# Optimization experiments

Measured on AMD Instinct MI355X. Metric: run time of the kernel, lower is better.

## Reference

```python
import jax, jax.numpy as jnp
import numpy as np

NUM_LAYERS = 2


def setup_inputs() -> dict:
    key = jax.random.key(0)
    ks = jax.random.split(key, 8)
    B, S, I, H = 64, 512, 64, 512
    def lin(kw, kb, fan_in, fan_out):
        bound = 1.0 / np.sqrt(fan_in)
        W = jax.random.uniform(kw, (fan_in, fan_out), jnp.float32, -bound, bound)
        b = jax.random.uniform(kb, (fan_out,), jnp.float32, -bound, bound)
        return W, b
    W0, b0 = lin(ks[0], ks[1], I + H, 4 * H)      # layer 0: cat(x_t, h0) -> gates
    W1, b1 = lin(ks[2], ks[3], H + H, 4 * H)      # layer 1: cat(h0, h1) -> gates
    Wfc, bfc = lin(ks[4], ks[5], H, 1)            # output head
    x = jax.random.normal(ks[6], (B, S, I), jnp.float32)
    return {"x": x, "W0": W0, "b0": b0, "W1": W1, "b1": b1, "Wfc": Wfc, "bfc": bfc}


def _lstm_cell(inp, h, c, W, b):
    gates = jnp.concatenate([inp, h], axis=1) @ W + b   # [B, 4H]
    i, f, g, o = jnp.split(gates, 4, axis=1)             # torch chunk order: i,f,g,o
    c_next = jax.nn.sigmoid(f) * c + jax.nn.sigmoid(i) * jnp.tanh(g)
    h_next = jax.nn.sigmoid(o) * jnp.tanh(c_next)
    return h_next, c_next


def reference(x, W0, b0, W1, b1, Wfc, bfc):
    B, S, _ = x.shape
    H = W0.shape[1] // 4
    Ws, bs = (W0, W1), (b0, b1)
    h0 = jnp.zeros((NUM_LAYERS, B, H), x.dtype)
    c0 = jnp.zeros((NUM_LAYERS, B, H), x.dtype)

    def step(carry, xt):
        h, c = carry
        hs, cs = [], []
        inp = xt
        for l in range(NUM_LAYERS):
            hn, cn = _lstm_cell(inp, h[l], c[l], Ws[l], bs[l])
            hs.append(hn); cs.append(cn)
            inp = hn
        return (jnp.stack(hs), jnp.stack(cs)), None

    (h_fin, _), _ = jax.lax.scan(step, (h0, c0), jnp.swapaxes(x, 0, 1))
    # original applies fc to every timestep then keeps only the last ->
    # equivalent to fc on final top-layer hidden state
    pred = h_fin[-1] @ Wfc + bfc    # [B, 1]
    return pred[:, 0]               # squeeze -> [B]
```

## Files before the change

kernel.cpp:

```cpp
#include <hip/hip_runtime.h>

#define S_LEN 512
#define HID   512
#define IN_D  64
#define GATES 2048
#define K0    576
#define K1    1024
#define KP0   578
#define KP1   1026
#define CLUSTERS 4
#define WGS   64
#define BPC   16
#define NBLOCKS 256
#define NTHREADS 256
#define NPROD 128u

typedef _Float16 f16;
typedef _Float16 f16x8 __attribute__((ext_vector_type(8)));
typedef float    f32x4 __attribute__((ext_vector_type(4)));

#define LDS_W0_OFF  0
#define LDS_W1_OFF  (32 * KP0 * 2)
#define LDS_STG_OFF (LDS_W1_OFF + 32 * KP1 * 2)
#define LDS_TOTAL   (LDS_STG_OFF + 4 * 16 * 17 * 4)

#define WS_FLAG_BYTES 65536
#define SLOT_BYTES    32768

#define RELEASE_DRAIN() asm volatile("s_waitcnt vmcnt(0) lgkmcnt(0)" ::: "memory")
#define MFMA(a,b,c) __builtin_amdgcn_mfma_f32_16x16x32_f16((a),(b),(c),0,0,0)

__device__ __forceinline__ float sigf(float v) {
  v = fminf(fmaxf(v, -30.f), 30.f);
  return 1.f / (1.f + __expf(-v));
}
__device__ __forceinline__ float tanh_f(float v) {
  v = fminf(fmaxf(v, -15.f), 15.f);
  float e = __expf(2.f * v);
  return (e - 1.f) / (e + 1.f);
}

__device__ __forceinline__ void wait_cnt(const unsigned* p, unsigned need, int& budget) {
  for (;;) {
    unsigned v = __hip_atomic_load(p, __ATOMIC_RELAXED, __HIP_MEMORY_SCOPE_AGENT);
    if (v >= need) break;
    if (--budget < 0) break;
    __builtin_amdgcn_s_sleep(1);
  }
  asm volatile("" ::: "memory");
}

extern "C" __global__ void __launch_bounds__(NTHREADS, 1)
lstm_persist(const float* __restrict__ x,  const float* __restrict__ W0,
             const float* __restrict__ b0, const float* __restrict__ W1,
             const float* __restrict__ b1, const float* __restrict__ Wfc,
             const float* __restrict__ bfc, float* __restrict__ out,
             unsigned char* __restrict__ ws, int Wn, int wmask, int fimask, int slack)
{
  extern __shared__ char lds[];
  f16*   w0l     = (f16*)(lds + LDS_W0_OFF);
  f16*   w1l     = (f16*)(lds + LDS_W1_OFF);
  float* stgbase = (float*)(lds + LDS_STG_OFF);

  const int tid   = threadIdx.x;
  const int wg    = blockIdx.x & (WGS - 1);
  const int cl    = blockIdx.x / WGS;
  const int wave  = tid >> 6;
  const int lane  = tid & 63;
  const int hbase = wg * 8;

  {
    const int nl = tid & 31;
    const int wtile = nl >> 4, wi = nl & 15, g = wi >> 2, jj = wi & 3;
    const int col = g * HID + hbase + wtile * 4 + jj;
    for (int k = tid >> 5; k < K0; k += 8)
      w0l[nl * KP0 + k] = (f16)W0[(size_t)k * GATES + col];
    for (int k = tid >> 5; k < K1; k += 8)
      w1l[nl * KP1 + k] = (f16)W1[(size_t)k * GATES + col];
  }
  __syncthreads();

  const int layer = wave >> 1;
  const int tile  = wave & 1;
  const int cb    = hbase + tile * 4;
  const int erow  = lane >> 2;
  const int ehc   = lane & 3;
  const int hcol  = cb + ehc;
  const float* bsrc = layer ? b1 : b0;
  const float bg0 = bsrc[0 * HID + hcol];
  const float bg1 = bsrc[1 * HID + hcol];
  const float bg2 = bsrc[2 * HID + hcol];
  const float bg3 = bsrc[3 * HID + hcol];
  float cstate = 0.f;
  float* stg = stgbase + wave * (16 * 17);

  const int fm  = lane & 15;
  const int q8  = (lane >> 4) * 8;
  const int brow = cl * BPC + fm;

  unsigned char* hby = ws + WS_FLAG_BYTES;
  unsigned int* f0cnt = (unsigned int*)(ws + (size_t)cl * 8192);
  unsigned int* f1cnt = (unsigned int*)(ws + (size_t)cl * 8192 + 2048);
  int budget = 1 << 20;

  auto slotp = [&](int lyr, int t, int hl) -> f16* {
    return (f16*)(hby + ((size_t)((cl * 2 + lyr) * Wn + (t & wmask)) << 15) + (hl << 14));
  };

  auto do_epilogue = [&](f32x4 acc, int t) {
    #pragma unroll
    for (int r = 0; r < 4; ++r)
      stg[((lane >> 4) * 4 + r) * 17 + fm] = acc[r];
    float iv = stg[erow * 17 + 0 + ehc]  + bg0;
    float fv = stg[erow * 17 + 4 + ehc]  + bg1;
    float gv = stg[erow * 17 + 8 + ehc]  + bg2;
    float ov = stg[erow * 17 + 12 + ehc] + bg3;
    float ig = sigf(iv), fg = sigf(fv), gg = tanh_f(gv), og = sigf(ov);
    cstate = fg * cstate + ig * gg;
    float h = og * tanh_f(cstate);

    const int src0 = fm * 4 + ((lane >> 4) & 1) * 2;
    float ha = __shfl(h, src0, 64);
    float hb = __shfl(h, src0 + 1, 64);
    if (lane < 32) {
      const int wrow = lane & 15, wpair = lane >> 4;
      f16* phi = slotp(layer, t, 0);
      f16* plo = slotp(layer, t, 1);
      f16 hah = (f16)ha; f16 hal = (f16)(ha - (float)hah);
      f16 hbh = (f16)hb; f16 hbl = (f16)(hb - (float)hbh);
      unsigned int hw = (unsigned int)__builtin_bit_cast(unsigned short, hah) |
                        ((unsigned int)__builtin_bit_cast(unsigned short, hbh) << 16);
      unsigned int lw = (unsigned int)__builtin_bit_cast(unsigned short, hal) |
                        ((unsigned int)__builtin_bit_cast(unsigned short, hbl) << 16);
      const int coff = wrow * HID + cb + wpair * 2;
      __hip_atomic_store((unsigned int*)(phi + coff), hw, __ATOMIC_RELAXED, __HIP_MEMORY_SCOPE_AGENT);
      __hip_atomic_store((unsigned int*)(plo + coff), lw, __ATOMIC_RELAXED, __HIP_MEMORY_SCOPE_AGENT);
    }
    RELEASE_DRAIN();
  };

  if (layer == 0) {
    for (int t = 0; t < S_LEN; ++t) {
      if (t && (t & fimask) == 0)
        __builtin_amdgcn_fence(__ATOMIC_ACQUIRE, "agent");
      f32x4 acc = {0.f, 0.f, 0.f, 0.f};
      const float* xr = x + ((size_t)brow * S_LEN + t) * IN_D + q8;
      #pragma unroll
      for (int kb = 0; kb < 2; ++kb) {
        f32x4 xa = *(const f32x4*)(xr + kb * 32);
        f32x4 xb = *(const f32x4*)(xr + kb * 32 + 4);
        f16x8 a = { (f16)xa[0], (f16)xa[1], (f16)xa[2], (f16)xa[3],
                    (f16)xb[0], (f16)xb[1], (f16)xb[2], (f16)xb[3] };
        f16x8 bf = *(const f16x8*)(w0l + (tile * 16 + fm) * KP0 + kb * 32 + q8);
        acc = MFMA(a, bf, acc);
      }
      if (t) {
        wait_cnt(f0cnt + (t - 1), NPROD, budget);
        if (t > slack) wait_cnt(f1cnt + (t - slack - 1), NPROD, budget);
        const f16* hpi = slotp(0, t - 1, 0) + fm * HID + q8;
        const f16* hpl = slotp(0, t - 1, 1) + fm * HID + q8;
        f16x8 ah[16], al[16];
        #pragma unroll
        for (int kb = 0; kb < 16; ++kb) {
          ah[kb] = *(const f16x8*)(hpi + kb * 32);
          al[kb] = *(const f16x8*)(hpl + kb * 32);
        }
        f32x4 acl = {0.f, 0.f, 0.f, 0.f};
        #pragma unroll
        for (int kb = 0; kb < 16; ++kb) {
          f16x8 bf = *(const f16x8*)(w0l + (tile * 16 + fm) * KP0 + IN_D + kb * 32 + q8);
          acc = MFMA(ah[kb], bf, acc);
          acl = MFMA(al[kb], bf, acl);
        }
        acc = acc + acl;
      }
      do_epilogue(acc, t);
      if (lane == 0) atomicAdd(f0cnt + t, 1u);
    }
  } else {
    for (int t = 0; t < S_LEN; ++t) {
      if (t && (t & fimask) == 0)
        __builtin_amdgcn_fence(__ATOMIC_ACQUIRE, "agent");
      f32x4 acc = {0.f, 0.f, 0.f, 0.f};
      f32x4 acl = {0.f, 0.f, 0.f, 0.f};
      wait_cnt(f0cnt + t, NPROD, budget);
      {
        const f16* h0i = slotp(0, t, 0) + fm * HID + q8;
        const f16* h0l = slotp(0, t, 1) + fm * HID + q8;
        f16x8 ah[16], al[16];
        #pragma unroll
        for (int kb = 0; kb < 16; ++kb) {
          ah[kb] = *(const f16x8*)(h0i + kb * 32);
          al[kb] = *(const f16x8*)(h0l + kb * 32);
        }
        #pragma unroll
        for (int kb = 0; kb < 16; ++kb) {
          f16x8 bf = *(const f16x8*)(w1l + (tile * 16 + fm) * KP1 + kb * 32 + q8);
          acc = MFMA(ah[kb], bf, acc);
          acl = MFMA(al[kb], bf, acl);
        }
      }
      if (t) {
        wait_cnt(f1cnt + (t - 1), NPROD, budget);
        const f16* h1i = slotp(1, t - 1, 0) + fm * HID + q8;
        const f16* h1l = slotp(1, t - 1, 1) + fm * HID + q8;
        f16x8 ah[16], al[16];
        #pragma unroll
        for (int kb = 0; kb < 16; ++kb) {
          ah[kb] = *(const f16x8*)(h1i + kb * 32);
          al[kb] = *(const f16x8*)(h1l + kb * 32);
        }
        #pragma unroll
        for (int kb = 0; kb < 16; ++kb) {
          f16x8 bf = *(const f16x8*)(w1l + (tile * 16 + fm) * KP1 + HID + kb * 32 + q8);
          acc = MFMA(ah[kb], bf, acc);
          acl = MFMA(al[kb], bf, acl);
        }
      }
      acc = acc + acl;
      do_epilogue(acc, t);
      if (lane == 0) atomicAdd(f1cnt + t, 1u);
    }
  }

  if (wg == 0) {
    wait_cnt(f1cnt + (S_LEN - 1), NPROD, budget);
    __builtin_amdgcn_fence(__ATOMIC_ACQUIRE, "agent");
    const f16* h1i = slotp(1, S_LEN - 1, 0);
    const f16* h1l = slotp(1, S_LEN - 1, 1);
    #pragma unroll
    for (int rr = 0; rr < 4; ++rr) {
      const int r = wave * 4 + rr;
      float sum = 0.f;
      for (int k = lane; k < HID; k += 64) {
        float hv = (float)h1i[r * HID + k] + (float)h1l[r * HID + k];
        sum += hv * Wfc[k];
      }
      #pragma unroll
      for (int off = 32; off > 0; off >>= 1)
        sum += __shfl_down(sum, off, 64);
      if (lane == 0) out[cl * BPC + r] = sum + bfc[0];
    }
  }
}

extern "C" void kernel_launch(void* const* d_in, const int* in_sizes, int n_in,
                              void* d_out, int out_size, void* d_ws, size_t ws_size,
                              hipStream_t stream) {
  const float* x   = (const float*)d_in[0];
  const float* W0  = (const float*)d_in[1];
  const float* b0  = (const float*)d_in[2];
  const float* W1  = (const float*)d_in[3];
  const float* b1  = (const float*)d_in[4];
  const float* Wfc = (const float*)d_in[5];
  const float* bfc = (const float*)d_in[6];
  float* out = (float*)d_out;
  unsigned char* ws = (unsigned char*)d_ws;

  (void)in_sizes; (void)n_in; (void)out_size;

  int Wn = 2;
  while (Wn < 64 &&
         WS_FLAG_BYTES + (size_t)(Wn * 2) * (CLUSTERS * 2 * SLOT_BYTES) <= ws_size)
    Wn *= 2;
  int wmask  = Wn - 1;
  int fimask = (Wn >= 4) ? (Wn / 2 - 1) : 0;
  int slack  = Wn - 2;

  hipFuncSetAttribute((const void*)lstm_persist,
                      hipFuncAttributeMaxDynamicSharedMemorySize, LDS_TOTAL);

  hipMemsetAsync(ws, 0, WS_FLAG_BYTES, stream);

  void* args[] = { &x, &W0, &b0, &W1, &b1, &Wfc, &bfc, &out, &ws,
                   &Wn, &wmask, &fimask, &slack };
  hipLaunchCooperativeKernel((void*)lstm_persist, dim3(NBLOCKS), dim3(NTHREADS),
                             args, LDS_TOTAL, stream);
}
```

Before: 5.185 ms.

## Stripe step counters across four words and merge layer-1 waits and loads

Each per-step arrival counter is split into four 32-bit words, and producers are spread over them by workgroup/tile id. This reduces atomic contention on a single address, and consumers poll all four with two 64-bit loads. Layer 1 now waits for both the layer-0 and its own previous-step flags before issuing all h loads at once and running four independent MFMA accumulator chains. Layer 0 polls its two dependencies in one combined loop. In exchange, the flag workspace per cluster doubles, layer 1 can no longer start its h0 MFMAs before h1 is ready, and register pressure rises from holding 64 vectors.

Result: slower. 6.364 ms (+22.7%).

```diff
diff --git a/kernel.cpp b/kernel.cpp
--- a/kernel.cpp
+++ b/kernel.cpp
@@ -13,7 +13,7 @@
 #define BPC   16
 #define NBLOCKS 256
 #define NTHREADS 256
-#define NPROD 128u
+#define NEED_W 32u
 
 typedef _Float16 f16;
 typedef _Float16 f16x8 __attribute__((ext_vector_type(8)));
@@ -40,10 +40,39 @@
   return (e - 1.f) / (e + 1.f);
 }
 
-__device__ __forceinline__ void wait_cnt(const unsigned* p, unsigned need, int& budget) {
+__device__ __forceinline__ bool cnt4_ok(unsigned long long a, unsigned long long b) {
+  return ((unsigned)a >= NEED_W) && ((unsigned)(a >> 32) >= NEED_W) &&
+         ((unsigned)b >= NEED_W) && ((unsigned)(b >> 32) >= NEED_W);
+}
+
+__device__ __forceinline__ void wait_cnt4(const unsigned* p, int& budget) {
+  const unsigned long long* q = (const unsigned long long*)p;
   for (;;) {
-    unsigned v = __hip_atomic_load(p, __ATOMIC_RELAXED, __HIP_MEMORY_SCOPE_AGENT);
-    if (v >= need) break;
+    unsigned long long a = __hip_atomic_load(q,     __ATOMIC_RELAXED, __HIP_MEMORY_SCOPE_AGENT);
+    unsigned long long b = __hip_atomic_load(q + 1, __ATOMIC_RELAXED, __HIP_MEMORY_SCOPE_AGENT);
+    if (cnt4_ok(a, b)) break;
+    if (--budget < 0) break;
+    __builtin_amdgcn_s_sleep(1);
+  }
+  asm volatile("" ::: "memory");
+}
+
+__device__ __forceinline__ void wait_cnt4_both(const unsigned* p0, const unsigned* p1, int& budget) {
+  const unsigned long long* q0 = (const unsigned long long*)p0;
+  const unsigned long long* q1 = (const unsigned long long*)p1;
+  bool d0 = false, d1 = false;
+  for (;;) {
+    if (!d0) {
+      unsigned long long a = __hip_atomic_load(q0,     __ATOMIC_RELAXED, __HIP_MEMORY_SCOPE_AGENT);
+      unsigned long long b = __hip_atomic_load(q0 + 1, __ATOMIC_RELAXED, __HIP_MEMORY_SCOPE_AGENT);
+      d0 = cnt4_ok(a, b);
+    }
+    if (!d1) {
+      unsigned long long a = __hip_atomic_load(q1,     __ATOMIC_RELAXED, __HIP_MEMORY_SCOPE_AGENT);
+      unsigned long long b = __hip_atomic_load(q1 + 1, __ATOMIC_RELAXED, __HIP_MEMORY_SCOPE_AGENT);
+      d1 = cnt4_ok(a, b);
+    }
+    if (d0 && d1) break;
     if (--budget < 0) break;
     __builtin_amdgcn_s_sleep(1);
   }
@@ -97,10 +126,12 @@
   const int fm  = lane & 15;
   const int q8  = (lane >> 4) * 8;
   const int brow = cl * BPC + fm;
+  const int wid  = wg * 2 + tile;
+  const int word = wid & 3;
 
   unsigned char* hby = ws + WS_FLAG_BYTES;
-  unsigned int* f0cnt = (unsigned int*)(ws + (size_t)cl * 8192);
-  unsigned int* f1cnt = (unsigned int*)(ws + (size_t)cl * 8192 + 2048);
+  unsigned int* f0cnt = (unsigned int*)(ws + (size_t)cl * 16384);
+  unsigned int* f1cnt = (unsigned int*)(ws + (size_t)cl * 16384 + 8192);
   int budget = 1 << 20;
 
   auto slotp = [&](int lyr, int t, int hl) -> f16* {
@@ -155,8 +186,10 @@
         acc = MFMA(a, bf, acc);
       }
       if (t) {
-        wait_cnt(f0cnt + (t - 1), NPROD, budget);
-        if (t > slack) wait_cnt(f1cnt + (t - slack - 1), NPROD, budget);
+        if (t > slack)
+          wait_cnt4_both(f0cnt + (t - 1) * 4, f1cnt + (t - slack - 1) * 4, budget);
+        else
+          wait_cnt4(f0cnt + (t - 1) * 4, budget);
         const f16* hpi = slotp(0, t - 1, 0) + fm * HID + q8;
         const f16* hpl = slotp(0, t - 1, 1) + fm * HID + q8;
         f16x8 ah[16], al[16];
@@ -175,56 +208,65 @@
         acc = acc + acl;
       }
       do_epilogue(acc, t);
-      if (lane == 0) atomicAdd(f0cnt + t, 1u);
+      if (lane == 0) atomicAdd(f0cnt + t * 4 + word, 1u);
     }
   } else {
     for (int t = 0; t < S_LEN; ++t) {
       if (t && (t & fimask) == 0)
         __builtin_amdgcn_fence(__ATOMIC_ACQUIRE, "agent");
-      f32x4 acc = {0.f, 0.f, 0.f, 0.f};
-      f32x4 acl = {0.f, 0.f, 0.f, 0.f};
-      wait_cnt(f0cnt + t, NPROD, budget);
+      if (t)
+        wait_cnt4_both(f0cnt + t * 4, f1cnt + (t - 1) * 4, budget);
+      else
+        wait_cnt4(f0cnt, budget);
+
+      f32x4 a0 = {0.f,0.f,0.f,0.f}, a1 = {0.f,0.f,0.f,0.f};
+      f32x4 a2 = {0.f,0.f,0.f,0.f}, a3 = {0.f,0.f,0.f,0.f};
       {
         const f16* h0i = slotp(0, t, 0) + fm * HID + q8;
         const f16* h0l = slotp(0, t, 1) + fm * HID + q8;
-        f16x8 ah[16], al[16];
-        #pragma unroll
-        for (int kb = 0; kb < 16; ++kb) {
-          ah[kb] = *(const f16x8*)(h0i + kb * 32);
-          al[kb] = *(const f16x8*)(h0l + kb * 32);
-        }
-        #pragma unroll
-        for (int kb = 0; kb < 16; ++kb) {
-          f16x8 bf = *(const f16x8*)(w1l + (tile * 16 + fm) * KP1 + kb * 32 + q8);
-          acc = MFMA(ah[kb], bf, acc);
-          acl = MFMA(al[kb], bf, acl);
+        if (t) {
+          const f16* h1i = slotp(1, t - 1, 0) + fm * HID + q8;
+          const f16* h1l = slotp(1, t - 1, 1) + fm * HID + q8;
+          f16x8 ah0[16], al0[16], ah1[16], al1[16];
+          #pragma unroll
+          for (int kb = 0; kb < 16; ++kb) {
+            ah0[kb] = *(const f16x8*)(h0i + kb * 32);
+            al0[kb] = *(const f16x8*)(h0l + kb * 32);
+            ah1[kb] = *(const f16x8*)(h1i + kb * 32);
+            al1[kb] = *(const f16x8*)(h1l + kb * 32);
+          }
+          #pragma unroll
+          for (int kb = 0; kb < 16; ++kb) {
+            f16x8 bf0 = *(const f16x8*)(w1l + (tile * 16 + fm) * KP1 + kb * 32 + q8);
+            f16x8 bf1 = *(const f16x8*)(w1l + (tile * 16 + fm) * KP1 + HID + kb * 32 + q8);
+            a0 = MFMA(ah0[kb], bf0, a0);
+            a1 = MFMA(al0[kb], bf0, a1);
+            a2 = MFMA(ah1[kb], bf1, a2);
+            a3 = MFMA(al1[kb], bf1, a3);
+          }
+        } else {
+          f16x8 ah0[16], al0[16];
+          #pragma unroll
+          for (int kb = 0; kb < 16; ++kb) {
+            ah0[kb] = *(const f16x8*)(h0i + kb * 32);
+            al0[kb] = *(const f16x8*)(h0l + kb * 32);
+          }
+          #pragma unroll
+          for (int kb = 0; kb < 16; ++kb) {
+            f16x8 bf0 = *(const f16x8*)(w1l + (tile * 16 + fm) * KP1 + kb * 32 + q8);
+            a0 = MFMA(ah0[kb], bf0, a0);
+            a1 = MFMA(al0[kb], bf0, a1);
+          }
         }
       }
-      if (t) {
-        wait_cnt(f1cnt + (t - 1), NPROD, budget);
-        const f16* h1i = slotp(1, t - 1, 0) + fm * HID + q8;
-        const f16* h1l = slotp(1, t - 1, 1) + fm * HID + q8;
-        f16x8 ah[16], al[16];
-        #pragma unroll
-        for (int kb = 0; kb < 16; ++kb) {
-          ah[kb] = *(const f16x8*)(h1i + kb * 32);
-          al[kb] = *(const f16x8*)(h1l + kb * 32);
-        }
-        #pragma unroll
-        for (int kb = 0; kb < 16; ++kb) {
-          f16x8 bf = *(const f16x8*)(w1l + (tile * 16 + fm) * KP1 + HID + kb * 32 + q8);
-          acc = MFMA(ah[kb], bf, acc);
-          acl = MFMA(al[kb], bf, acl);
-        }
-      }
-      acc = acc + acl;
+      f32x4 acc = (a0 + a1) + (a2 + a3);
       do_epilogue(acc, t);
-      if (lane == 0) atomicAdd(f1cnt + t, 1u);
+      if (lane == 0) atomicAdd(f1cnt + t * 4 + word, 1u);
     }
   }
 
   if (wg == 0) {
-    wait_cnt(f1cnt + (S_LEN - 1), NPROD, budget);
+    wait_cnt4(f1cnt + (S_LEN - 1) * 4, budget);
     __builtin_amdgcn_fence(__ATOMIC_ACQUIRE, "agent");
     const f16* h1i = slotp(1, S_LEN - 1, 0);
     const f16* h1l = slotp(1, S_LEN - 1, 1);
```
